# Kernel optimization log

Measured on AMD Instinct MI355X. Metric: run time of the kernel, lower is better.

Reference implementation:

```python
import jax, jax.numpy as jnp
import numpy as np
import math

EMBED_DIM = 1024
NUM_HEADS = 16
HEAD_DIM = EMBED_DIM // NUM_HEADS
ACT_BITS = 8
WGT_BITS = 8


def fake_quant(x, n_bits):
    # Per-tensor symmetric fake quantization with straight-through estimator.
    qmax = 2.0 ** (n_bits - 1) - 1.0  # 127 for 8 bits
    scale = jnp.maximum(jnp.max(jnp.abs(x)) / qmax, 1e-8)
    q = jnp.clip(jnp.round(x / scale), -qmax - 1.0, qmax) * scale
    return x + jax.lax.stop_gradient(q - x)


def setup_inputs() -> dict:
    key = jax.random.key(0)
    ks = jax.random.split(key, 7)
    S, B, D = 2048, 2, EMBED_DIM
    return {
        "query": jax.random.normal(ks[0], (S, B, D), dtype=jnp.float32),
        "key": jax.random.normal(ks[1], (S, B, D), dtype=jnp.float32),
        "value": jax.random.normal(ks[2], (S, B, D), dtype=jnp.float32),
        "Wi": jax.random.normal(ks[3], (3 * D, D), dtype=jnp.float32) * (1.0 / math.sqrt(D)),
        "bi": jax.random.normal(ks[4], (3 * D,), dtype=jnp.float32) * 0.01,
        "Wo": jax.random.normal(ks[5], (D, D), dtype=jnp.float32) * (1.0 / math.sqrt(D)),
        "bo": jax.random.normal(ks[6], (D,), dtype=jnp.float32) * 0.01,
    }


def reference(query, key, value, Wi, bi, Wo, bo):
    D, H, hd = EMBED_DIM, NUM_HEADS, HEAD_DIM
    len_q, batch, _ = query.shape
    len_k = key.shape[0]

    Wi_q = fake_quant(Wi, WGT_BITS)
    Wo_q = fake_quant(Wo, WGT_BITS)

    # in-projections (full 3D projection per input, then chunk, as in source)
    Xq = fake_quant(query @ Wi_q.T + bi, ACT_BITS)
    Xk = fake_quant(key @ Wi_q.T + bi, ACT_BITS)
    Xv = fake_quant(value @ Wi_q.T + bi, ACT_BITS)
    Q = Xq[..., :D]
    K = Xk[..., D:2 * D]
    V = Xv[..., 2 * D:]

    # [len, B, D] -> [B*H, len, hd]
    q = Q.reshape(len_q, batch * H, hd).transpose(1, 0, 2)
    k = K.reshape(len_k, batch * H, hd).transpose(1, 0, 2)
    v = V.reshape(len_k, batch * H, hd).transpose(1, 0, 2)

    q = fake_quant(q / math.sqrt(hd), ACT_BITS)
    attn = jnp.einsum('bqd,bkd->bqk', q, k)  # note: attn/softmax fake-quants in source are no-ops (result discarded)
    attn = jax.nn.softmax(attn, axis=-1)
    heads = fake_quant(jnp.einsum('bqk,bkd->bqd', attn, v), ACT_BITS)

    # [B*H, len_q, hd] -> [len_q*B, D]
    heads_reshape = heads.transpose(1, 0, 2).reshape(len_q * batch, D)
    y = (heads_reshape @ Wo_q.T + bo).reshape(len_q, batch, D)
    return fake_quant(y, ACT_BITS)
```

## Files before the change

### kernel.cpp

```cpp
#include <hip/hip_runtime.h>
#include <math.h>


typedef _Float16 f16;
typedef _Float16 half8 __attribute__((ext_vector_type(8)));
typedef _Float16 half4 __attribute__((ext_vector_type(4)));
typedef _Float16 half2v __attribute__((ext_vector_type(2)));
typedef __fp16 fp16x2 __attribute__((ext_vector_type(2)));
typedef float floatx4 __attribute__((ext_vector_type(4)));
typedef int int4v __attribute__((ext_vector_type(4)));

#define QMAX 127.0f

#define SLOT_WI 0
#define SLOT_WO 1
#define SLOT_XQ 2
#define SLOT_XK 3
#define SLOT_XV 4
#define SLOT_HD 5
#define SLOT_Y  6
#define SLOT_Q  7

__device__ __forceinline__ float slot_scale(const unsigned* slots, int slot, float premul) {
  if (slot < 0) return 1.0f;
  return fmaxf(__uint_as_float(slots[slot]) * premul / QMAX, 1e-8f);
}

__device__ __forceinline__ void gl2lds16(const void* gsrc, void* ldst) {
  __builtin_amdgcn_global_load_lds((__attribute__((address_space(1))) void*)gsrc,
                                   (__attribute__((address_space(3))) void*)ldst, 16, 0, 0);
}

__device__ __forceinline__ half2v pack2(float a, float b) {
  fp16x2 r = __builtin_amdgcn_cvt_pkrtz(a, b);
  return __builtin_bit_cast(half2v, r);
}

__global__ __launch_bounds__(64) void init_slots_k(unsigned* slots) {
  if (threadIdx.x < 16) slots[threadIdx.x] = 0u;
}

__global__ __launch_bounds__(256) void absmax2_k(const float* __restrict__ Wi,
                                                 const float* __restrict__ Wo,
                                                 unsigned* __restrict__ slots) {
  __shared__ float red[256];
  int tid = threadIdx.x;
  const float4* x4;
  int n4, i0, stride, slot;
  if (blockIdx.x < 768) {
    x4 = (const float4*)Wi; n4 = 786432; i0 = blockIdx.x * 256 + tid;
    stride = 768 * 256; slot = SLOT_WI;
  } else {
    x4 = (const float4*)Wo; n4 = 262144; i0 = (blockIdx.x - 768) * 256 + tid;
    stride = 256 * 256; slot = SLOT_WO;
  }
  float lmax = 0.f;
  for (int i = i0; i < n4; i += stride) {
    float4 v = x4[i];
    lmax = fmaxf(lmax, fmaxf(fmaxf(fabsf(v.x), fabsf(v.y)), fmaxf(fabsf(v.z), fabsf(v.w))));
  }
  red[tid] = lmax; __syncthreads();
  for (int sh = 128; sh > 0; sh >>= 1) {
    if (tid < sh) red[tid] = fmaxf(red[tid], red[tid + sh]);
    __syncthreads();
  }
  if (tid == 0) atomicMax(&slots[slot], __float_as_uint(red[0]));
}

__global__ __launch_bounds__(256) void quantw_k(const float* __restrict__ Wi,
                                                const float* __restrict__ Wo,
                                                f16* __restrict__ Wiq,
                                                char* __restrict__ Wo8,
                                                const unsigned* __restrict__ slots) {
  int tid = threadIdx.x;
  if (blockIdx.x < 768) {
    float s = slot_scale(slots, SLOT_WI, 1.0f);
    const float4* in4 = (const float4*)Wi;
    for (int i = blockIdx.x * 256 + tid; i < 786432; i += 768 * 256) {
      float4 v = in4[i];
      float xs[4] = {v.x, v.y, v.z, v.w};
      half4 o;
#pragma unroll
      for (int u = 0; u < 4; ++u) {
        float r = rintf(xs[u] / s);
        o[u] = (f16)fminf(fmaxf(r, -128.0f), 127.0f);
      }
      *(half4*)(Wiq + (size_t)i * 4) = o;
    }
  } else {
    float s = slot_scale(slots, SLOT_WO, 1.0f);
    const float4* in4 = (const float4*)Wo;
    for (int i = (blockIdx.x - 768) * 256 + tid; i < 262144; i += 256 * 256) {
      float4 v = in4[i];
      char4 o;
      o.x = (signed char)(int)fminf(fmaxf(rintf(v.x / s), -128.0f), 127.0f);
      o.y = (signed char)(int)fminf(fmaxf(rintf(v.y / s), -128.0f), 127.0f);
      o.z = (signed char)(int)fminf(fmaxf(rintf(v.z / s), -128.0f), 127.0f);
      o.w = (signed char)(int)fminf(fmaxf(rintf(v.w / s), -128.0f), 127.0f);
      *(char4*)(Wo8 + (size_t)i * 4) = o;
    }
  }
}

__global__ __launch_bounds__(256) void quantf_k(const float* __restrict__ in, float* __restrict__ out,
                                                int n4, unsigned* __restrict__ slots,
                                                int sSlot, float premul) {
  float s = slot_scale(slots, sSlot, premul);
  const float4* in4 = (const float4*)in;
  float4* out4 = (float4*)out;
  for (int i = blockIdx.x * 256 + threadIdx.x; i < n4; i += gridDim.x * 256) {
    float4 v = in4[i];
    float xs[4] = {v.x, v.y, v.z, v.w};
#pragma unroll
    for (int u = 0; u < 4; ++u) {
      float r = rintf((xs[u] * premul) / s);
      r = fminf(fmaxf(r, -128.0f), 127.0f);
      xs[u] = r * s;
    }
    out4[i] = make_float4(xs[0], xs[1], xs[2], xs[3]);
  }
}

__global__ __launch_bounds__(256) void quanti_k(const float* __restrict__ in, f16* __restrict__ out,
                                                int n4, unsigned* __restrict__ slots,
                                                int sSlot, int outAbsSlot) {
  __shared__ float red[256];
  float s = slot_scale(slots, sSlot, 1.0f);
  float lmax = 0.f;
  const float4* in4 = (const float4*)in;
  for (int i = blockIdx.x * 256 + threadIdx.x; i < n4; i += gridDim.x * 256) {
    float4 v = in4[i];
    float xs[4] = {v.x, v.y, v.z, v.w};
    half4 o;
#pragma unroll
    for (int u = 0; u < 4; ++u) {
      float r = rintf(xs[u] / s);
      r = fminf(fmaxf(r, -128.0f), 127.0f);
      o[u] = (f16)r;
      lmax = fmaxf(lmax, fabsf(r));
    }
    *(half4*)(out + (size_t)i * 4) = o;
  }
  if (outAbsSlot >= 0) {
    int tid = threadIdx.x;
    red[tid] = lmax; __syncthreads();
    for (int sh = 128; sh > 0; sh >>= 1) {
      if (tid < sh) red[tid] = fmaxf(red[tid], red[tid + sh]);
      __syncthreads();
    }
    if (tid == 0) atomicMax(&slots[outAbsSlot], __float_as_uint(red[0] * s));
  }
}

__global__ __launch_bounds__(256) void quant8_k(const float* __restrict__ in, char* __restrict__ out,
                                                int n4, const unsigned* __restrict__ slots,
                                                int sSlot) {
  float s = slot_scale(slots, sSlot, 1.0f);
  const float4* in4 = (const float4*)in;
  for (int i = blockIdx.x * 256 + threadIdx.x; i < n4; i += gridDim.x * 256) {
    float4 v = in4[i];
    char4 o;
    o.x = (signed char)(int)fminf(fmaxf(rintf(v.x / s), -128.0f), 127.0f);
    o.y = (signed char)(int)fminf(fmaxf(rintf(v.y / s), -128.0f), 127.0f);
    o.z = (signed char)(int)fminf(fmaxf(rintf(v.z / s), -128.0f), 127.0f);
    o.w = (signed char)(int)fminf(fmaxf(rintf(v.w / s), -128.0f), 127.0f);
    *(char4*)(out + (size_t)i * 4) = o;
  }
}

__global__ __launch_bounds__(256) void split_k(const float* __restrict__ in,
                                               f16* __restrict__ hi, f16* __restrict__ lo, int n4) {
  const float4* in4 = (const float4*)in;
  for (int i = blockIdx.x * 256 + threadIdx.x; i < n4; i += gridDim.x * 256) {
    float4 v = in4[i];
    float xs[4] = {v.x, v.y, v.z, v.w};
    half4 h, l;
#pragma unroll
    for (int u = 0; u < 4; ++u) {
      f16 hv = (f16)xs[u];
      h[u] = hv;
      l[u] = (f16)(xs[u] - (float)hv);
    }
    *(half4*)(hi + (size_t)i * 4) = h;
    *(half4*)(lo + (size_t)i * 4) = l;
  }
}

__global__ __launch_bounds__(256) void quantv_t_k(const float* __restrict__ Xv,
                                                  f16* __restrict__ Vt,
                                                  const unsigned* __restrict__ slots) {
  __shared__ f16 T[64][68];
  int tid = threadIdx.x;
  int bh = blockIdx.y, b = bh >> 4, h = bh & 15;
  int k0 = blockIdx.x * 64;
  float s = slot_scale(slots, SLOT_XV, 1.0f);
#pragma unroll
  for (int it = 0; it < 4; ++it) {
    int idx = tid + it * 256;
    int row = idx >> 4, dseg = idx & 15;
    float4 v = *(const float4*)(Xv + ((size_t)(k0 + row) * 2 + b) * 1024 + h * 64 + dseg * 4);
    float xs[4] = {v.x, v.y, v.z, v.w};
    half4 o;
#pragma unroll
    for (int u = 0; u < 4; ++u) {
      float r = rintf(xs[u] / s);
      o[u] = (f16)fminf(fmaxf(r, -128.0f), 127.0f);
    }
    *(half4*)&T[row][dseg * 4] = o;
  }
  __syncthreads();
#pragma unroll
  for (int it = 0; it < 2; ++it) {
    int sdx = tid + it * 256;
    int d = sdx >> 3, j8 = sdx & 7;
    half8 o;
#pragma unroll
    for (int l = 0; l < 8; ++l) {
      int pos = j8 * 8 + l;
      int tp = pos >> 5, pq = (pos & 31) >> 3, jj = pos & 7;
      int k = tp * 32 + pq * 4 + ((jj < 4) ? jj : jj + 12);
      o[l] = T[k][d];
    }
    *(half8*)(Vt + ((size_t)bh * 64 + d) * 2048 + k0 + j8 * 8) = o;
  }
}

__global__ __launch_bounds__(256) void gemm_mfma_k(const f16* __restrict__ A0,
                                                   const f16* __restrict__ A1,
                                                   const f16* __restrict__ B,
                                                   const float* __restrict__ bias,
                                                   float* __restrict__ out,
                                                   unsigned* __restrict__ slots,
                                                   int slotB, int absSlot,
                                                   int K, int colLo, int colCount) {
  __shared__ f16 AsH[128 * 32];
  __shared__ f16 Bs[128 * 32];
  __shared__ f16 AsL[128 * 32];
  __shared__ float red[256];

  int tid = threadIdx.x;
  int lane = tid & 63, w = tid >> 6;
  int wm = w >> 1, wn = w & 1;
  int quad = lane >> 4, l15 = lane & 15;
  int m0 = blockIdx.y * 128, n0 = blockIdx.x * 128;

  int srow = lane >> 2;
  int sgr = (lane & 3) * 8;

  floatx4 acc[4][4];
#pragma unroll
  for (int i = 0; i < 4; ++i)
#pragma unroll
    for (int j = 0; j < 4; ++j) acc[i][j] = (floatx4){0.f, 0.f, 0.f, 0.f};

  for (int k0 = 0; k0 < K; k0 += 32) {
    __syncthreads();
#pragma unroll
    for (int t = 0; t < 2; ++t) {
      int r0 = (w * 2 + t) * 16;
      gl2lds16(A0 + (size_t)(m0 + r0 + srow) * K + k0 + sgr, &AsH[r0 * 32]);
      gl2lds16(B + (size_t)(n0 + r0 + srow) * K + k0 + sgr, &Bs[r0 * 32]);
      gl2lds16(A1 + (size_t)(m0 + r0 + srow) * K + k0 + sgr, &AsL[r0 * 32]);
    }
    __syncthreads();
    half8 ah[4], bfr[4], al[4];
#pragma unroll
    for (int i = 0; i < 4; ++i) ah[i] = *(half8*)&AsH[(wm * 64 + i * 16 + l15) * 32 + quad * 8];
#pragma unroll
    for (int j = 0; j < 4; ++j) bfr[j] = *(half8*)&Bs[(wn * 64 + j * 16 + l15) * 32 + quad * 8];
#pragma unroll
    for (int i = 0; i < 4; ++i) al[i] = *(half8*)&AsL[(wm * 64 + i * 16 + l15) * 32 + quad * 8];
#pragma unroll
    for (int i = 0; i < 4; ++i)
#pragma unroll
      for (int j = 0; j < 4; ++j) {
        acc[i][j] = __builtin_amdgcn_mfma_f32_16x16x32_f16(ah[i], bfr[j], acc[i][j], 0, 0, 0);
        acc[i][j] = __builtin_amdgcn_mfma_f32_16x16x32_f16(al[i], bfr[j], acc[i][j], 0, 0, 0);
      }
  }

  float sc = slot_scale(slots, slotB, 1.0f);
  float lmax = 0.f;
#pragma unroll
  for (int i = 0; i < 4; ++i) {
#pragma unroll
    for (int j = 0; j < 4; ++j) {
      int gn = n0 + wn * 64 + j * 16 + l15;
      float bv = bias[gn];
#pragma unroll
      for (int r = 0; r < 4; ++r) {
        int gm = m0 + wm * 64 + i * 16 + quad * 4 + r;
        float v = acc[i][j][r] * sc + bv;
        lmax = fmaxf(lmax, fabsf(v));
        if (gn >= colLo && gn < colLo + colCount)
          out[(size_t)gm * colCount + (gn - colLo)] = v;
      }
    }
  }
  red[tid] = lmax; __syncthreads();
  for (int sh = 128; sh > 0; sh >>= 1) {
    if (tid < sh) red[tid] = fmaxf(red[tid], red[tid + sh]);
    __syncthreads();
  }
  if (tid == 0) atomicMax(&slots[absSlot], __float_as_uint(red[0]));
}

__global__ __launch_bounds__(256) void gemm_i8out_k(const char* __restrict__ A8,
                                                    const char* __restrict__ B8,
                                                    const float* __restrict__ bias,
                                                    float* __restrict__ out,
                                                    unsigned* __restrict__ slots) {
  __shared__ char As8[128 * 64];
  __shared__ char Bs8[128 * 64];
  __shared__ float red[256];

  const int K = 1024;
  int tid = threadIdx.x;
  int lane = tid & 63, w = tid >> 6;
  int wm = w >> 1, wn = w & 1;
  int quad = lane >> 4, l15 = lane & 15;
  int m0 = blockIdx.y * 128, n0 = blockIdx.x * 128;

  int srow = lane >> 2;
  int sgr = (lane & 3) * 16;

  int4v acc[4][4];
#pragma unroll
  for (int i = 0; i < 4; ++i)
#pragma unroll
    for (int j = 0; j < 4; ++j) acc[i][j] = (int4v){0, 0, 0, 0};

  for (int k0 = 0; k0 < K; k0 += 64) {
    __syncthreads();
#pragma unroll
    for (int t = 0; t < 2; ++t) {
      int r0 = (w * 2 + t) * 16;
      int row = r0 + srow;
      gl2lds16(A8 + (size_t)(m0 + row) * K + k0 + sgr, &As8[r0 * 64]);
      gl2lds16(B8 + (size_t)(n0 + row) * K + k0 + sgr, &Bs8[r0 * 64]);
    }
    __syncthreads();
    int4v af[4], bf[4];
#pragma unroll
    for (int i = 0; i < 4; ++i)
      af[i] = *(const int4v*)&As8[(wm * 64 + i * 16 + l15) * 64 + quad * 16];
#pragma unroll
    for (int j = 0; j < 4; ++j)
      bf[j] = *(const int4v*)&Bs8[(wn * 64 + j * 16 + l15) * 64 + quad * 16];
#pragma unroll
    for (int i = 0; i < 4; ++i)
#pragma unroll
      for (int j = 0; j < 4; ++j)
        acc[i][j] = __builtin_amdgcn_mfma_i32_16x16x64_i8(af[i], bf[j], acc[i][j], 0, 0, 0);
  }

  float sc = slot_scale(slots, SLOT_HD, 1.0f) * slot_scale(slots, SLOT_WO, 1.0f);
  float lmax = 0.f;
#pragma unroll
  for (int i = 0; i < 4; ++i) {
#pragma unroll
    for (int j = 0; j < 4; ++j) {
      int gn = n0 + wn * 64 + j * 16 + l15;
      float bv = bias[gn];
#pragma unroll
      for (int r = 0; r < 4; ++r) {
        int gm = m0 + wm * 64 + i * 16 + quad * 4 + r;
        float v = (float)acc[i][j][r] * sc + bv;
        lmax = fmaxf(lmax, fabsf(v));
        out[(size_t)gm * 1024 + gn] = v;
      }
    }
  }
  red[tid] = lmax; __syncthreads();
  for (int sh = 128; sh > 0; sh >>= 1) {
    if (tid < sh) red[tid] = fmaxf(red[tid], red[tid + sh]);
    __syncthreads();
  }
  if (tid == 0) atomicMax(&slots[SLOT_Y], __float_as_uint(red[0]));
}

__global__ __launch_bounds__(256) void attn_k(const f16* __restrict__ Qc,
                                              const f16* __restrict__ Kh,
                                              const f16* __restrict__ Vt,
                                              float* __restrict__ heads,
                                              unsigned* __restrict__ slots) {
  __shared__ f16 Ks[64 * 64];
  __shared__ f16 Vs[64][72];
  __shared__ float lred[4][2][16];
  __shared__ float red[256];

  int tid = threadIdx.x;
  int lane = tid & 63, w = tid >> 6;
  int quad = lane >> 4, l15 = lane & 15;
  int bh = blockIdx.y, b = bh >> 4, h = bh & 15;
  int q0 = blockIdx.x * 128;

  float s1 = slot_scale(slots, SLOT_XQ, 1.0f);
  float sq = slot_scale(slots, SLOT_Q, 0.125f);
  float sk = slot_scale(slots, SLOT_XK, 1.0f);
  float sv = slot_scale(slots, SLOT_XV, 1.0f);
  float cS = sq * sk * 1.44269504088896340736f;
  const float FOFF = 12.0f;

  half8 qf[2][2];
#pragma unroll
  for (int s = 0; s < 2; ++s) {
    const f16* qrow = Qc + ((size_t)(q0 + w * 32 + s * 16 + l15) * 2 + b) * 1024 + h * 64;
    half8 qr0 = *(const half8*)(qrow + quad * 8);
    half8 qr1 = *(const half8*)(qrow + 32 + quad * 8);
#pragma unroll
    for (int u = 0; u < 8; ++u) {
      float x0 = ((float)qr0[u] * s1) * 0.125f;
      float x1 = ((float)qr1[u] * s1) * 0.125f;
      qf[s][0][u] = (f16)fminf(fmaxf(rintf(x0 / sq), -128.0f), 127.0f);
      qf[s][1][u] = (f16)fminf(fmaxf(rintf(x1 / sq), -128.0f), 127.0f);
    }
  }

  int ksrow = lane >> 3;
  int ksp = lane & 7;
  int vr0 = tid >> 3, vs0 = (tid & 7) * 8;

  floatx4 oacc[2][4];
#pragma unroll
  for (int s = 0; s < 2; ++s)
#pragma unroll
    for (int d = 0; d < 4; ++d) oacc[s][d] = (floatx4){0.f, 0.f, 0.f, 0.f};
  float lsum[2] = {0.f, 0.f};

  const f16* vbase = Vt + (size_t)bh * 131072;

  for (int kt = 0; kt < 2048; kt += 64) {
    __syncthreads();
#pragma unroll
    for (int t = 0; t < 2; ++t) {
      int r0 = (w * 2 + t) * 8;
      int row = r0 + ksrow;
      int g = ksp ^ (row & 7);
      gl2lds16(Kh + ((size_t)(kt + row) * 2 + b) * 1024 + h * 64 + g * 8, &Ks[r0 * 64]);
    }
    half8 va = *(const half8*)(vbase + (size_t)vr0 * 2048 + kt + vs0);
    half8 vb = *(const half8*)(vbase + (size_t)(vr0 + 32) * 2048 + kt + vs0);
    *(half8*)&Vs[vr0][vs0] = va;
    *(half8*)&Vs[vr0 + 32][vs0] = vb;
    __syncthreads();

    half8 aph[2][2], apl[2][2];
#pragma unroll
    for (int t = 0; t < 4; ++t) {
      int row = t * 16 + l15;
      int g1 = quad ^ (row & 7);
      half8 kf0 = *(half8*)&Ks[row * 64 + g1 * 8];
      half8 kf1 = *(half8*)&Ks[row * 64 + (g1 ^ 4) * 8];
      int tp = t >> 1, hi = (t & 1) * 4;
#pragma unroll
      for (int s = 0; s < 2; ++s) {
        floatx4 sacc = (floatx4){0.f, 0.f, 0.f, 0.f};
        sacc = __builtin_amdgcn_mfma_f32_16x16x32_f16(kf0, qf[s][0], sacc, 0, 0, 0);
        sacc = __builtin_amdgcn_mfma_f32_16x16x32_f16(kf1, qf[s][1], sacc, 0, 0, 0);
        float p0 = __builtin_amdgcn_exp2f(fmaf(sacc[0], cS, -FOFF));
        float p1 = __builtin_amdgcn_exp2f(fmaf(sacc[1], cS, -FOFF));
        float p2 = __builtin_amdgcn_exp2f(fmaf(sacc[2], cS, -FOFF));
        float p3 = __builtin_amdgcn_exp2f(fmaf(sacc[3], cS, -FOFF));
        lsum[s] += (p0 + p1) + (p2 + p3);
        half2v h01 = pack2(p0, p1);
        half2v h23 = pack2(p2, p3);
        half2v l01 = pack2(p0 - (float)h01[0], p1 - (float)h01[1]);
        half2v l23 = pack2(p2 - (float)h23[0], p3 - (float)h23[1]);
        aph[s][tp][hi + 0] = h01[0]; aph[s][tp][hi + 1] = h01[1];
        aph[s][tp][hi + 2] = h23[0]; aph[s][tp][hi + 3] = h23[1];
        apl[s][tp][hi + 0] = l01[0]; apl[s][tp][hi + 1] = l01[1];
        apl[s][tp][hi + 2] = l23[0]; apl[s][tp][hi + 3] = l23[1];
      }
    }

#pragma unroll
    for (int d = 0; d < 4; ++d) {
      const f16* vsrow = &Vs[d * 16 + l15][0];
      half8 b0 = *(const half8*)(vsrow + quad * 8);
      half8 b1 = *(const half8*)(vsrow + 32 + quad * 8);
#pragma unroll
      for (int s = 0; s < 2; ++s) {
        oacc[s][d] = __builtin_amdgcn_mfma_f32_16x16x32_f16(aph[s][0], b0, oacc[s][d], 0, 0, 0);
        oacc[s][d] = __builtin_amdgcn_mfma_f32_16x16x32_f16(apl[s][0], b0, oacc[s][d], 0, 0, 0);
        oacc[s][d] = __builtin_amdgcn_mfma_f32_16x16x32_f16(aph[s][1], b1, oacc[s][d], 0, 0, 0);
        oacc[s][d] = __builtin_amdgcn_mfma_f32_16x16x32_f16(apl[s][1], b1, oacc[s][d], 0, 0, 0);
      }
    }
  }

#pragma unroll
  for (int s = 0; s < 2; ++s) {
    float l = lsum[s];
    l += __shfl_xor(l, 16);
    l += __shfl_xor(l, 32);
    lred[w][s][l15] = l;
  }
  float linv[2][4];
#pragma unroll
  for (int s = 0; s < 2; ++s)
#pragma unroll
    for (int r = 0; r < 4; ++r) linv[s][r] = sv / lred[w][s][quad * 4 + r];

  float lmax = 0.f;
#pragma unroll
  for (int s = 0; s < 2; ++s)
#pragma unroll
    for (int d = 0; d < 4; ++d)
#pragma unroll
      for (int r = 0; r < 4; ++r) {
        float hv = oacc[s][d][r] * linv[s][r];
        heads[((size_t)(q0 + w * 32 + s * 16 + quad * 4 + r) * 2 + b) * 1024 +
              h * 64 + d * 16 + l15] = hv;
        lmax = fmaxf(lmax, fabsf(hv));
      }
  red[tid] = lmax; __syncthreads();
  for (int sh = 128; sh > 0; sh >>= 1) {
    if (tid < sh) red[tid] = fmaxf(red[tid], red[tid + sh]);
    __syncthreads();
  }
  if (tid == 0) atomicMax(&slots[SLOT_HD], __float_as_uint(red[0]));
}

extern "C" void kernel_launch(void* const* d_in, const int* in_sizes, int n_in,
                              void* d_out, int out_size, void* d_ws, size_t ws_size,
                              hipStream_t stream) {
  (void)in_sizes; (void)n_in; (void)out_size; (void)ws_size;
  const float* query = (const float*)d_in[0];
  const float* key   = (const float*)d_in[1];
  const float* value = (const float*)d_in[2];
  const float* Wi    = (const float*)d_in[3];
  const float* bi    = (const float*)d_in[4];
  const float* Wo    = (const float*)d_in[5];
  const float* bo    = (const float*)d_in[6];
  float* out = (float*)d_out;

  char* p = (char*)d_ws;
  unsigned* slots = (unsigned*)p;            p += 1024;
  f16* Wiq  = (f16*)p;                       p += 3072 * 1024 * 2;
  char* Wo8 = (char*)p;                      p += 1024 * 1024;
  f16* Ahi  = (f16*)p;                       p += 4096 * 1024 * 2;
  f16* Alo  = (f16*)p;                       p += 4096 * 1024 * 2;
  float* Hd = (float*)Ahi;
  float* Xq = (float*)p;                     p += 4096 * 1024 * 4;
  float* Y  = Xq;
  float* Xk = (float*)p;                     p += 4096 * 1024 * 4;
  f16* Qc   = (f16*)Xk;
  float* Xv = (float*)p;                     p += 4096 * 1024 * 4;
  char* Hint8 = (char*)Xv + 4096 * 1024 * 2;
  f16* Kint = (f16*)p;                       p += 4096 * 1024 * 2;
  f16* Vt   = (f16*)p;                       p += 4096 * 1024 * 2;

  init_slots_k<<<1, 64, 0, stream>>>(slots);
  absmax2_k<<<1024, 256, 0, stream>>>(Wi, Wo, slots);
  quantw_k<<<1024, 256, 0, stream>>>(Wi, Wo, Wiq, Wo8, slots);

  dim3 g1(24, 32);
  split_k<<<1024, 256, 0, stream>>>(query, Ahi, Alo, 1048576);
  gemm_mfma_k<<<g1, 256, 0, stream>>>(Ahi, Alo, Wiq, bi, Xq, slots, SLOT_WI, SLOT_XQ,
                                      1024, 0, 1024);
  split_k<<<1024, 256, 0, stream>>>(key, Ahi, Alo, 1048576);
  gemm_mfma_k<<<g1, 256, 0, stream>>>(Ahi, Alo, Wiq, bi, Xk, slots, SLOT_WI, SLOT_XK,
                                      1024, 1024, 1024);
  split_k<<<1024, 256, 0, stream>>>(value, Ahi, Alo, 1048576);
  gemm_mfma_k<<<g1, 256, 0, stream>>>(Ahi, Alo, Wiq, bi, Xv, slots, SLOT_WI, SLOT_XV,
                                      1024, 2048, 1024);

  quanti_k<<<1024, 256, 0, stream>>>(Xk, Kint, 1048576, slots, SLOT_XK, -1);
  quanti_k<<<1024, 256, 0, stream>>>(Xq, Qc, 1048576, slots, SLOT_XQ, SLOT_Q);

  dim3 gvt(32, 32);
  quantv_t_k<<<gvt, 256, 0, stream>>>(Xv, Vt, slots);

  dim3 ga(16, 32);
  attn_k<<<ga, 256, 0, stream>>>(Qc, Kint, Vt, Hd, slots);

  quant8_k<<<1024, 256, 0, stream>>>(Hd, Hint8, 1048576, slots, SLOT_HD);

  dim3 g2(8, 32);
  gemm_i8out_k<<<g2, 256, 0, stream>>>(Hint8, Wo8, bo, Y, slots);

  quantf_k<<<1024, 256, 0, stream>>>(Y, out, 1048576, slots, SLOT_Y, 1.0f);
}
```

Measured before the change: 437.3 us.

## Replace fp16 hi/lo split QKV projection with int8 two-digit MFMA GEMM

The fp32 query, key and value activations are now quantized to a 15-bit grid using a global absmax and split into two signed int8 digits. The three in-projections are merged into a single launch that runs int8 MFMA (16x16x64) against int8 weights. This replaces two fp16 MFMAs per tile with two int8 MFMAs that cover twice the K depth, and it removes the separate split kernels. The cost is an extra absmax pass over the inputs and some approximation error from quantizing the activations to about 14 bits, which could slightly change results near rounding boundaries.

New measurement: 444.8 us. Within noise of the previous version (+1.7%).

```diff
diff --git a/kernel.cpp b/kernel.cpp
--- a/kernel.cpp
+++ b/kernel.cpp
@@ -20,12 +20,17 @@
 #define SLOT_HD 5
 #define SLOT_Y  6
 #define SLOT_Q  7
+#define SLOT_A  8
 
 __device__ __forceinline__ float slot_scale(const unsigned* slots, int slot, float premul) {
   if (slot < 0) return 1.0f;
   return fmaxf(__uint_as_float(slots[slot]) * premul / QMAX, 1e-8f);
 }
 
+__device__ __forceinline__ float slot_scaleA(const unsigned* slots) {
+  return fmaxf(__uint_as_float(slots[SLOT_A]) / 16256.0f, 1e-8f);
+}
+
 __device__ __forceinline__ void gl2lds16(const void* gsrc, void* ldst) {
   __builtin_amdgcn_global_load_lds((__attribute__((address_space(1))) void*)gsrc,
                                    (__attribute__((address_space(3))) void*)ldst, 16, 0, 0);
@@ -40,24 +45,34 @@
   if (threadIdx.x < 16) slots[threadIdx.x] = 0u;
 }
 
-__global__ __launch_bounds__(256) void absmax2_k(const float* __restrict__ Wi,
+__global__ __launch_bounds__(256) void absmax3_k(const float* __restrict__ Wi,
                                                  const float* __restrict__ Wo,
+                                                 const float* __restrict__ q,
+                                                 const float* __restrict__ k,
+                                                 const float* __restrict__ v,
                                                  unsigned* __restrict__ slots) {
   __shared__ float red[256];
   int tid = threadIdx.x;
+  int bid = blockIdx.x;
   const float4* x4;
   int n4, i0, stride, slot;
-  if (blockIdx.x < 768) {
-    x4 = (const float4*)Wi; n4 = 786432; i0 = blockIdx.x * 256 + tid;
+  if (bid < 768) {
+    x4 = (const float4*)Wi; n4 = 786432; i0 = bid * 256 + tid;
     stride = 768 * 256; slot = SLOT_WI;
+  } else if (bid < 1024) {
+    x4 = (const float4*)Wo; n4 = 262144; i0 = (bid - 768) * 256 + tid;
+    stride = 256 * 256; slot = SLOT_WO;
   } else {
-    x4 = (const float4*)Wo; n4 = 262144; i0 = (blockIdx.x - 768) * 256 + tid;
-    stride = 256 * 256; slot = SLOT_WO;
+    int r = bid - 1024;
+    int t = r >> 9;
+    x4 = (const float4*)(t == 0 ? q : (t == 1 ? k : v));
+    n4 = 1048576; i0 = (r & 511) * 256 + tid;
+    stride = 512 * 256; slot = SLOT_A;
   }
   float lmax = 0.f;
   for (int i = i0; i < n4; i += stride) {
-    float4 v = x4[i];
-    lmax = fmaxf(lmax, fmaxf(fmaxf(fabsf(v.x), fabsf(v.y)), fmaxf(fabsf(v.z), fabsf(v.w))));
+    float4 vv = x4[i];
+    lmax = fmaxf(lmax, fmaxf(fmaxf(fabsf(vv.x), fabsf(vv.y)), fmaxf(fabsf(vv.z), fabsf(vv.w))));
   }
   red[tid] = lmax; __syncthreads();
   for (int sh = 128; sh > 0; sh >>= 1) {
@@ -69,7 +84,7 @@
 
 __global__ __launch_bounds__(256) void quantw_k(const float* __restrict__ Wi,
                                                 const float* __restrict__ Wo,
-                                                f16* __restrict__ Wiq,
+                                                char* __restrict__ Wi8,
                                                 char* __restrict__ Wo8,
                                                 const unsigned* __restrict__ slots) {
   int tid = threadIdx.x;
@@ -78,14 +93,12 @@
     const float4* in4 = (const float4*)Wi;
     for (int i = blockIdx.x * 256 + tid; i < 786432; i += 768 * 256) {
       float4 v = in4[i];
-      float xs[4] = {v.x, v.y, v.z, v.w};
-      half4 o;
-#pragma unroll
-      for (int u = 0; u < 4; ++u) {
-        float r = rintf(xs[u] / s);
-        o[u] = (f16)fminf(fmaxf(r, -128.0f), 127.0f);
-      }
-      *(half4*)(Wiq + (size_t)i * 4) = o;
+      char4 o;
+      o.x = (signed char)(int)fminf(fmaxf(rintf(v.x / s), -128.0f), 127.0f);
+      o.y = (signed char)(int)fminf(fmaxf(rintf(v.y / s), -128.0f), 127.0f);
+      o.z = (signed char)(int)fminf(fmaxf(rintf(v.z / s), -128.0f), 127.0f);
+      o.w = (signed char)(int)fminf(fmaxf(rintf(v.w / s), -128.0f), 127.0f);
+      *(char4*)(Wi8 + (size_t)i * 4) = o;
     }
   } else {
     float s = slot_scale(slots, SLOT_WO, 1.0f);
@@ -99,6 +112,33 @@
       o.w = (signed char)(int)fminf(fmaxf(rintf(v.w / s), -128.0f), 127.0f);
       *(char4*)(Wo8 + (size_t)i * 4) = o;
     }
+  }
+}
+
+__global__ __launch_bounds__(256) void digitize_k(const float* __restrict__ q,
+                                                  const float* __restrict__ k,
+                                                  const float* __restrict__ v,
+                                                  char* __restrict__ A1,
+                                                  char* __restrict__ A2,
+                                                  const unsigned* __restrict__ slots) {
+  float inv = 1.0f / slot_scaleA(slots);
+  char4* o1 = (char4*)A1;
+  char4* o2 = (char4*)A2;
+  for (int i = blockIdx.x * 256 + threadIdx.x; i < 3145728; i += gridDim.x * 256) {
+    int t = i >> 20;
+    const float4* src = (const float4*)(t == 0 ? q : (t == 1 ? k : v));
+    float4 x = src[i & 1048575];
+    float xs[4] = {x.x, x.y, x.z, x.w};
+    signed char c1s[4], c2s[4];
+#pragma unroll
+    for (int u = 0; u < 4; ++u) {
+      float qv = fminf(fmaxf(rintf(xs[u] * inv), -16256.0f), 16256.0f);
+      float c1 = rintf(qv * 0.0078125f);
+      c1s[u] = (signed char)(int)c1;
+      c2s[u] = (signed char)(int)(qv - 128.0f * c1);
+    }
+    o1[i] = make_char4(c1s[0], c1s[1], c1s[2], c1s[3]);
+    o2[i] = make_char4(c2s[0], c2s[1], c2s[2], c2s[3]);
   }
 }
 
@@ -168,24 +208,6 @@
   }
 }
 
-__global__ __launch_bounds__(256) void split_k(const float* __restrict__ in,
-                                               f16* __restrict__ hi, f16* __restrict__ lo, int n4) {
-  const float4* in4 = (const float4*)in;
-  for (int i = blockIdx.x * 256 + threadIdx.x; i < n4; i += gridDim.x * 256) {
-    float4 v = in4[i];
-    float xs[4] = {v.x, v.y, v.z, v.w};
-    half4 h, l;
-#pragma unroll
-    for (int u = 0; u < 4; ++u) {
-      f16 hv = (f16)xs[u];
-      h[u] = hv;
-      l[u] = (f16)(xs[u] - (float)hv);
-    }
-    *(half4*)(hi + (size_t)i * 4) = h;
-    *(half4*)(lo + (size_t)i * 4) = l;
-  }
-}
-
 __global__ __launch_bounds__(256) void quantv_t_k(const float* __restrict__ Xv,
                                                   f16* __restrict__ Vt,
                                                   const unsigned* __restrict__ slots) {
@@ -225,61 +247,72 @@
   }
 }
 
-__global__ __launch_bounds__(256) void gemm_mfma_k(const f16* __restrict__ A0,
-                                                   const f16* __restrict__ A1,
-                                                   const f16* __restrict__ B,
-                                                   const float* __restrict__ bias,
-                                                   float* __restrict__ out,
-                                                   unsigned* __restrict__ slots,
-                                                   int slotB, int absSlot,
-                                                   int K, int colLo, int colCount) {
-  __shared__ f16 AsH[128 * 32];
-  __shared__ f16 Bs[128 * 32];
-  __shared__ f16 AsL[128 * 32];
+__global__ __launch_bounds__(256) void gemm_qkv_i8_k(const char* __restrict__ A1,
+                                                     const char* __restrict__ A2,
+                                                     const char* __restrict__ B8,
+                                                     const float* __restrict__ bias,
+                                                     float* __restrict__ Xout,
+                                                     unsigned* __restrict__ slots) {
+  __shared__ char As1[128 * 64];
+  __shared__ char As2[128 * 64];
+  __shared__ char Bs8[128 * 64];
   __shared__ float red[256];
 
+  const int K = 1024;
   int tid = threadIdx.x;
   int lane = tid & 63, w = tid >> 6;
   int wm = w >> 1, wn = w & 1;
   int quad = lane >> 4, l15 = lane & 15;
-  int m0 = blockIdx.y * 128, n0 = blockIdx.x * 128;
+  int t = blockIdx.y >> 5;
+  int m0 = (blockIdx.y & 31) * 128;
+  int n0 = blockIdx.x * 128;
+  size_t aoff = (size_t)t * 4194304;
 
   int srow = lane >> 2;
-  int sgr = (lane & 3) * 8;
-
-  floatx4 acc[4][4];
+  int sgr = (lane & 3) * 16;
+
+  int4v acc1[4][4], acc2[4][4];
 #pragma unroll
   for (int i = 0; i < 4; ++i)
 #pragma unroll
-    for (int j = 0; j < 4; ++j) acc[i][j] = (floatx4){0.f, 0.f, 0.f, 0.f};
-
-  for (int k0 = 0; k0 < K; k0 += 32) {
-    __syncthreads();
-#pragma unroll
-    for (int t = 0; t < 2; ++t) {
-      int r0 = (w * 2 + t) * 16;
-      gl2lds16(A0 + (size_t)(m0 + r0 + srow) * K + k0 + sgr, &AsH[r0 * 32]);
-      gl2lds16(B + (size_t)(n0 + r0 + srow) * K + k0 + sgr, &Bs[r0 * 32]);
-      gl2lds16(A1 + (size_t)(m0 + r0 + srow) * K + k0 + sgr, &AsL[r0 * 32]);
-    }
-    __syncthreads();
-    half8 ah[4], bfr[4], al[4];
-#pragma unroll
-    for (int i = 0; i < 4; ++i) ah[i] = *(half8*)&AsH[(wm * 64 + i * 16 + l15) * 32 + quad * 8];
-#pragma unroll
-    for (int j = 0; j < 4; ++j) bfr[j] = *(half8*)&Bs[(wn * 64 + j * 16 + l15) * 32 + quad * 8];
-#pragma unroll
-    for (int i = 0; i < 4; ++i) al[i] = *(half8*)&AsL[(wm * 64 + i * 16 + l15) * 32 + quad * 8];
+    for (int j = 0; j < 4; ++j) {
+      acc1[i][j] = (int4v){0, 0, 0, 0};
+      acc2[i][j] = (int4v){0, 0, 0, 0};
+    }
+
+  for (int k0 = 0; k0 < K; k0 += 64) {
+    __syncthreads();
+#pragma unroll
+    for (int u = 0; u < 2; ++u) {
+      int r0 = (w * 2 + u) * 16;
+      int row = r0 + srow;
+      gl2lds16(A1 + aoff + (size_t)(m0 + row) * K + k0 + sgr, &As1[r0 * 64]);
+      gl2lds16(A2 + aoff + (size_t)(m0 + row) * K + k0 + sgr, &As2[r0 * 64]);
+      gl2lds16(B8 + (size_t)(n0 + row) * K + k0 + sgr, &Bs8[r0 * 64]);
+    }
+    __syncthreads();
+    int4v a1f[4], a2f[4], bf[4];
 #pragma unroll
     for (int i = 0; i < 4; ++i)
+      a1f[i] = *(const int4v*)&As1[(wm * 64 + i * 16 + l15) * 64 + quad * 16];
+#pragma unroll
+    for (int i = 0; i < 4; ++i)
+      a2f[i] = *(const int4v*)&As2[(wm * 64 + i * 16 + l15) * 64 + quad * 16];
+#pragma unroll
+    for (int j = 0; j < 4; ++j)
+      bf[j] = *(const int4v*)&Bs8[(wn * 64 + j * 16 + l15) * 64 + quad * 16];
+#pragma unroll
+    for (int i = 0; i < 4; ++i)
 #pragma unroll
       for (int j = 0; j < 4; ++j) {
-        acc[i][j] = __builtin_amdgcn_mfma_f32_16x16x32_f16(ah[i], bfr[j], acc[i][j], 0, 0, 0);
-        acc[i][j] = __builtin_amdgcn_mfma_f32_16x16x32_f16(al[i], bfr[j], acc[i][j], 0, 0, 0);
+        acc1[i][j] = __builtin_amdgcn_mfma_i32_16x16x64_i8(a1f[i], bf[j], acc1[i][j], 0, 0, 0);
+        acc2[i][j] = __builtin_amdgcn_mfma_i32_16x16x64_i8(a2f[i], bf[j], acc2[i][j], 0, 0, 0);
       }
   }
 
-  float sc = slot_scale(slots, slotB, 1.0f);
+  float sc = slot_scaleA(slots) * slot_scale(slots, SLOT_WI, 1.0f);
+  int colLo = t * 1024;
+  float* outT = Xout + aoff;
   float lmax = 0.f;
 #pragma unroll
   for (int i = 0; i < 4; ++i) {
@@ -287,13 +320,13 @@
     for (int j = 0; j < 4; ++j) {
       int gn = n0 + wn * 64 + j * 16 + l15;
       float bv = bias[gn];
+      bool wr = (gn >= colLo && gn < colLo + 1024);
 #pragma unroll
       for (int r = 0; r < 4; ++r) {
         int gm = m0 + wm * 64 + i * 16 + quad * 4 + r;
-        float v = acc[i][j][r] * sc + bv;
-        lmax = fmaxf(lmax, fabsf(v));
-        if (gn >= colLo && gn < colLo + colCount)
-          out[(size_t)gm * colCount + (gn - colLo)] = v;
+        float vv = fmaf((float)acc1[i][j][r], 128.0f, (float)acc2[i][j][r]) * sc + bv;
+        lmax = fmaxf(lmax, fabsf(vv));
+        if (wr) outT[(size_t)gm * 1024 + (gn - colLo)] = vv;
       }
     }
   }
@@ -302,7 +335,7 @@
     if (tid < sh) red[tid] = fmaxf(red[tid], red[tid + sh]);
     __syncthreads();
   }
-  if (tid == 0) atomicMax(&slots[absSlot], __float_as_uint(red[0]));
+  if (tid == 0) atomicMax(&slots[SLOT_XQ + t], __float_as_uint(red[0]));
 }
 
 __global__ __launch_bounds__(256) void gemm_i8out_k(const char* __restrict__ A8,
@@ -537,34 +570,27 @@
 
   char* p = (char*)d_ws;
   unsigned* slots = (unsigned*)p;            p += 1024;
-  f16* Wiq  = (f16*)p;                       p += 3072 * 1024 * 2;
-  char* Wo8 = (char*)p;                      p += 1024 * 1024;
-  f16* Ahi  = (f16*)p;                       p += 4096 * 1024 * 2;
-  f16* Alo  = (f16*)p;                       p += 4096 * 1024 * 2;
-  float* Hd = (float*)Ahi;
+  char* Wi8 = p;                             p += 3072 * 1024;
+  char* Wo8 = p;                             p += 1024 * 1024;
+  char* A1  = p;                             p += 12288 * 1024;
+  char* A2  = p;                             p += 12288 * 1024;
+  float* Hd = (float*)A1;
+  f16* Kint = (f16*)(A2 + 4194304);
   float* Xq = (float*)p;                     p += 4096 * 1024 * 4;
   float* Y  = Xq;
   float* Xk = (float*)p;                     p += 4096 * 1024 * 4;
   f16* Qc   = (f16*)Xk;
   float* Xv = (float*)p;                     p += 4096 * 1024 * 4;
   char* Hint8 = (char*)Xv + 4096 * 1024 * 2;
-  f16* Kint = (f16*)p;                       p += 4096 * 1024 * 2;
   f16* Vt   = (f16*)p;                       p += 4096 * 1024 * 2;
 
   init_slots_k<<<1, 64, 0, stream>>>(slots);
-  absmax2_k<<<1024, 256, 0, stream>>>(Wi, Wo, slots);
-  quantw_k<<<1024, 256, 0, stream>>>(Wi, Wo, Wiq, Wo8, slots);
-
-  dim3 g1(24, 32);
-  split_k<<<1024, 256, 0, stream>>>(query, Ahi, Alo, 1048576);
-  gemm_mfma_k<<<g1, 256, 0, stream>>>(Ahi, Alo, Wiq, bi, Xq, slots, SLOT_WI, SLOT_XQ,
-                                      1024, 0, 1024);
-  split_k<<<1024, 256, 0, stream>>>(key, Ahi, Alo, 1048576);
-  gemm_mfma_k<<<g1, 256, 0, stream>>>(Ahi, Alo, Wiq, bi, Xk, slots, SLOT_WI, SLOT_XK,
-                                      1024, 1024, 1024);
-  split_k<<<1024, 256, 0, stream>>>(value, Ahi, Alo, 1048576);
-  gemm_mfma_k<<<g1, 256, 0, stream>>>(Ahi, Alo, Wiq, bi, Xv, slots, SLOT_WI, SLOT_XV,
-                                      1024, 2048, 1024);
+  absmax3_k<<<2560, 256, 0, stream>>>(Wi, Wo, query, key, value, slots);
+  quantw_k<<<1024, 256, 0, stream>>>(Wi, Wo, Wi8, Wo8, slots);
+  digitize_k<<<2048, 256, 0, stream>>>(query, key, value, A1, A2, slots);
+
+  dim3 gq(24, 96);
+  gemm_qkv_i8_k<<<gq, 256, 0, stream>>>(A1, A2, Wi8, bi, Xq, slots);
 
   quanti_k<<<1024, 256, 0, stream>>>(Xk, Kint, 1048576, slots, SLOT_XK, -1);
   quanti_k<<<1024, 256, 0, stream>>>(Xq, Qc, 1048576, slots, SLOT_XQ, SLOT_Q);
```
